# Kernel tuning notes

Hardware: AMD Instinct MI355X
Metric: run time of the kernel (lower is better)

The kernel has to match this reference:

```python
import jax, jax.numpy as jnp
import numpy as np

B, S, T, H, E = 64, 256, 128, 1024, 512


def setup_inputs() -> dict:
    key = jax.random.key(0)
    ks = jax.random.split(key, 16)
    sc = 0.02
    inp = {
        "trg_embed": jax.random.normal(ks[0], (B, T, E), jnp.float32),
        "encoder_hidden": jax.random.normal(ks[1], (B, S, 2 * H), jnp.float32),
        "encoder_final": jax.random.normal(ks[2], (1, B, 2 * H), jnp.float32),
        "src_mask": jnp.ones((B, 1, S), dtype=bool),
        "trg_mask": jnp.ones((B, 1, T), dtype=bool),
        # bridge: Linear(2H -> H, bias)
        "W_bridge": jax.random.normal(ks[3], (H, 2 * H), jnp.float32) * sc,
        "b_bridge": jnp.zeros((H,), jnp.float32),
        # Bahdanau attention: key/query/energy layers (no bias)
        "W_key": jax.random.normal(ks[4], (H, 2 * H), jnp.float32) * sc,
        "W_query": jax.random.normal(ks[5], (H, H), jnp.float32) * sc,
        "v_energy": jax.random.normal(ks[6], (H,), jnp.float32) * sc,
        # GRU (1 layer): input size E + 2H, hidden H. PyTorch gate order [r, z, n].
        "W_ih": jax.random.normal(ks[7], (3 * H, E + 2 * H), jnp.float32) * sc,
        "W_hh": jax.random.normal(ks[8], (3 * H, H), jnp.float32) * sc,
        "b_ih": jnp.zeros((3 * H,), jnp.float32),
        "b_hh": jnp.zeros((3 * H,), jnp.float32),
        # pre_output: Linear(H + 2H + E -> H, no bias)
        "W_pre": jax.random.normal(ks[9], (H, H + 2 * H + E), jnp.float32) * sc,
    }
    return inp


def reference(trg_embed, encoder_hidden, encoder_final, src_mask, trg_mask,
              W_bridge, b_bridge, W_key, W_query, v_energy,
              W_ih, W_hh, b_ih, b_hh, W_pre):
    neg_inf = jnp.float32(-1e9)
    # init_hidden: tanh(bridge(encoder_final)) -> [num_layers, B, H]; take last layer
    h0 = jnp.tanh(jnp.einsum('lbk,hk->lbh', encoder_final, W_bridge) + b_bridge)[-1]  # [B, H]
    # precompute projected keys once (as in forward())
    proj_key = jnp.einsum('bsk,hk->bsh', encoder_hidden, W_key)  # [B, S, H]
    mask = src_mask[:, 0, :]  # [B, S]

    def step(h, prev_embed):  # h: [B,H], prev_embed: [B,E]
        # Bahdanau attention with query = last-layer hidden state
        q = h @ W_query.T                                        # [B, H]
        energies = jnp.tanh(q[:, None, :] + proj_key) @ v_energy  # [B, S]
        energies = jnp.where(mask, energies, neg_inf)
        alphas = jax.nn.softmax(energies, axis=-1)               # [B, S]
        context = jnp.einsum('bs,bsd->bd', alphas, encoder_hidden)  # [B, 2H]
        # GRU step on concat(prev_embed, context)
        x = jnp.concatenate([prev_embed, context], axis=-1)      # [B, E+2H]
        gi = x @ W_ih.T + b_ih                                   # [B, 3H]
        gh = h @ W_hh.T + b_hh                                   # [B, 3H]
        i_r, i_z, i_n = jnp.split(gi, 3, axis=-1)
        h_r, h_z, h_n = jnp.split(gh, 3, axis=-1)
        r = jax.nn.sigmoid(i_r + h_r)
        z = jax.nn.sigmoid(i_z + h_z)
        n = jnp.tanh(i_n + r * h_n)
        h_new = (1.0 - z) * n + z * h                            # [B, H]
        # pre-output projection (dropout disabled: eval / p effectively identity)
        pre = jnp.concatenate([prev_embed, h_new, context], axis=-1) @ W_pre.T  # [B, H]
        return h_new, (h_new, pre)

    h_final, (states, pres) = jax.lax.scan(step, h0, jnp.swapaxes(trg_embed, 0, 1))
    decoder_states = jnp.swapaxes(states, 0, 1)      # [B, T, H]
    pre_output_vectors = jnp.swapaxes(pres, 0, 1)    # [B, T, H]
    hidden = h_final[None]                            # [num_layers=1, B, H]
    return decoder_states, hidden, pre_output_vectors
```

## Files before the change

kernel.cpp:

```cpp
#include <hip/hip_runtime.h>

#define Bn 64
#define Sn 256
#define Tn 128
#define Hn 1024
#define En 512
#define H2n 2048
#define NBLK 256
#define NTHR 1024

#define WCTX 10
#define WH 12

#define GW 0
#define PWc 0
#define PWh 32768
#define PWq 49152
#define PWe 65536
#define PREP 73728
#define SCR2 75776
#define SCR 147456
#define GIL 155648
#define LDS_BYTES 161792

typedef __attribute__((ext_vector_type(8))) short short8v;
typedef __attribute__((ext_vector_type(4))) float floatx4;

__device__ __forceinline__ unsigned short f2bf(float f) {
  union { float f; unsigned u; } x; x.f = f;
  unsigned r = x.u + 0x7fffu + ((x.u >> 16) & 1u);
  return (unsigned short)(r >> 16);
}
__device__ __forceinline__ float bf2f(unsigned short u) {
  union { unsigned u; float f; } x; x.u = ((unsigned)u) << 16; return x.f;
}
__device__ __forceinline__ float sigm(float x) { return 1.f / (1.f + __expf(-x)); }
__device__ __forceinline__ float tanh_f(float x) {
  float e = __expf(2.f * x);
  return 1.f - 2.f / (e + 1.f);
}
__device__ __forceinline__ short8v ldf(const unsigned short* p) { return *(const short8v*)p; }
#define MFMA(a, b, c) __builtin_amdgcn_mfma_f32_16x16x32_bf16(a, b, c, 0, 0, 0)

__device__ __forceinline__ float ldc_f(const float* p) {
  return __hip_atomic_load(p, __ATOMIC_RELAXED, __HIP_MEMORY_SCOPE_AGENT);
}
__device__ __forceinline__ void stc_f(float* p, float v) {
  __hip_atomic_store(p, v, __ATOMIC_RELAXED, __HIP_MEMORY_SCOPE_AGENT);
}
__device__ __forceinline__ void stc_u32(unsigned* p, unsigned v) {
  __hip_atomic_store(p, v, __ATOMIC_RELAXED, __HIP_MEMORY_SCOPE_AGENT);
}
__device__ __forceinline__ unsigned long long ldc_u64(const unsigned long long* p) {
  return __hip_atomic_load(p, __ATOMIC_RELAXED, __HIP_MEMORY_SCOPE_AGENT);
}
__device__ __forceinline__ void stc_u64(unsigned long long* p, unsigned long long v) {
  __hip_atomic_store(p, v, __ATOMIC_RELAXED, __HIP_MEMORY_SCOPE_AGENT);
}

__device__ __forceinline__ void bar_lds() {
  __builtin_amdgcn_sched_barrier(0);
  asm volatile("s_waitcnt lgkmcnt(0)" ::: "memory");
  __builtin_amdgcn_s_barrier();
  __builtin_amdgcn_sched_barrier(0);
}

__device__ __forceinline__ short8v packf(const float* p) {
  float4 e0 = *(const float4*)p, e1 = *(const float4*)(p + 4);
  short8v x;
  x[0] = (short)f2bf(e0.x); x[1] = (short)f2bf(e0.y);
  x[2] = (short)f2bf(e0.z); x[3] = (short)f2bf(e0.w);
  x[4] = (short)f2bf(e1.x); x[5] = (short)f2bf(e1.y);
  x[6] = (short)f2bf(e1.z); x[7] = (short)f2bf(e1.w);
  return x;
}

__global__ __launch_bounds__(256) void cast_kernel(const float4* __restrict__ src,
                                                   uint2* __restrict__ dst, int n4) {
  for (int i = blockIdx.x * blockDim.x + threadIdx.x; i < n4; i += gridDim.x * blockDim.x) {
    float4 v = src[i];
    uint2 p;
    p.x = (unsigned)f2bf(v.x) | ((unsigned)f2bf(v.y) << 16);
    p.y = (unsigned)f2bf(v.z) | ((unsigned)f2bf(v.w) << 16);
    dst[i] = p;
  }
}

__global__ __launch_bounds__(256) void bridge_kernel(const float* __restrict__ ef,
                                                     const float* __restrict__ Wb,
                                                     const float* __restrict__ bb,
                                                     float* __restrict__ h0out,
                                                     unsigned short* __restrict__ hb0) {
  __shared__ float efs[H2n];
  const int b = blockIdx.x >> 2, jq = blockIdx.x & 3;
  const int j = jq * 256 + threadIdx.x;
  for (int i = threadIdx.x; i < H2n; i += 256) efs[i] = ef[(size_t)b * H2n + i];
  __syncthreads();
  const float* wr = Wb + (size_t)j * H2n;
  float acc = bb[j];
  for (int k = 0; k < H2n; k += 4) {
    float4 wv = *(const float4*)&wr[k];
    acc += efs[k] * wv.x + efs[k + 1] * wv.y + efs[k + 2] * wv.z + efs[k + 3] * wv.w;
  }
  float th = tanhf(acc);
  h0out[(size_t)b * Hn + j] = th;
  hb0[(size_t)b * Hn + j] = f2bf(th);
}

__global__ __launch_bounds__(256) void pk_gemm(const unsigned short* __restrict__ A,
                                               const unsigned short* __restrict__ Bw,
                                               unsigned short* __restrict__ pk) {
  const int bid = blockIdx.x;
  const int mt = bid >> 4, nt = bid & 15;
  const int w = threadIdx.x >> 6, lane = threadIdx.x & 63;
  const int lm = lane & 15, lk = lane >> 4, ko = lk * 8;
  const unsigned short* arow = A + (size_t)(mt * 64 + w * 16 + lm) * 2048 + ko;
  const unsigned short* b0 = Bw + (size_t)(nt * 64 + lm) * 2048 + ko;
  const unsigned short* b1 = Bw + (size_t)(nt * 64 + 16 + lm) * 2048 + ko;
  const unsigned short* b2 = Bw + (size_t)(nt * 64 + 32 + lm) * 2048 + ko;
  const unsigned short* b3 = Bw + (size_t)(nt * 64 + 48 + lm) * 2048 + ko;
  floatx4 c0 = {0,0,0,0}, c1 = {0,0,0,0}, c2 = {0,0,0,0}, c3 = {0,0,0,0};
  for (int k = 0; k < 2048; k += 32) {
    short8v a = ldf(arow + k);
    c0 = MFMA(a, ldf(b0 + k), c0);
    c1 = MFMA(a, ldf(b1 + k), c1);
    c2 = MFMA(a, ldf(b2 + k), c2);
    c3 = MFMA(a, ldf(b3 + k), c3);
  }
  const int m = mt * 64 + w * 16 + lk * 4;
  const int j = nt * 64 + lm;
#pragma unroll
  for (int r = 0; r < 4; ++r) {
    unsigned short* row = pk + (size_t)(m + r) * 1024 + j;
    row[0]  = f2bf(c0[r]);
    row[16] = f2bf(c1[r]);
    row[32] = f2bf(c2[r]);
    row[48] = f2bf(c3[r]);
  }
}

struct DA {
  const float* emb; const float* v; const float* bih; const float* bhh;
  const unsigned short* pk; const unsigned short* ehb;
  const unsigned short* Wih; const unsigned short* Whh;
  const unsigned short* Wpre; const unsigned short* Wq;
  float* hbuf; unsigned short* hbR; float* qbuf; float* wbuf; float* psump;
  unsigned short* ctxR; unsigned* bar; float* out;
};

__device__ __forceinline__ void gbar(unsigned* bar, int tid, unsigned idx, int inv) {
  asm volatile("s_waitcnt vmcnt(0)" ::: "memory");
  __syncthreads();
  if (tid == 0) {
    unsigned old = __hip_atomic_fetch_add(bar, 1u, __ATOMIC_RELAXED, __HIP_MEMORY_SCOPE_AGENT);
    if (old + 1u == (unsigned)NBLK * idx) {
      __hip_atomic_store(bar + 32, idx, __ATOMIC_RELAXED, __HIP_MEMORY_SCOPE_AGENT);
    } else {
      unsigned g;
      do {
        __builtin_amdgcn_s_sleep(2);
        g = __hip_atomic_load(bar + 32, __ATOMIC_RELAXED, __HIP_MEMORY_SCOPE_AGENT);
      } while (g < idx);
    }
  }
  __syncthreads();
  if (inv) __builtin_amdgcn_fence(__ATOMIC_ACQUIRE, "agent");
}

__device__ __forceinline__ void gbar_pk(const DA& a, unsigned* bar, int tid, unsigned idx,
                                        int inv, int b, int sc4, int w, int lane,
                                        short8v* pkr) {
  asm volatile("s_waitcnt vmcnt(0)" ::: "memory");
  __syncthreads();
  __builtin_amdgcn_sched_barrier(0);
#pragma unroll
  for (int i = 0; i < 4; ++i) {
    const unsigned short* prow =
        a.pk + ((size_t)b * Sn + sc4 * 64 + w * 4 + i) * Hn + lane * 16;
    pkr[i] = ldf(prow);
    pkr[4 + i] = ldf(prow + 8);
  }
  __builtin_amdgcn_sched_barrier(0);
  if (tid == 0) {
    unsigned old = __hip_atomic_fetch_add(bar, 1u, __ATOMIC_RELAXED, __HIP_MEMORY_SCOPE_AGENT);
    if (old + 1u == (unsigned)NBLK * idx) {
      __hip_atomic_store(bar + 32, idx, __ATOMIC_RELAXED, __HIP_MEMORY_SCOPE_AGENT);
    } else {
      unsigned g;
      do {
        __builtin_amdgcn_s_sleep(2);
        g = __hip_atomic_load(bar + 32, __ATOMIC_RELAXED, __HIP_MEMORY_SCOPE_AGENT);
      } while (g < idx);
    }
  }
  __syncthreads();
  if (inv) __builtin_amdgcn_fence(__ATOMIC_ACQUIRE, "agent");
}

__device__ __forceinline__ void gateC_signal(unsigned* bar, int tid) {
  asm volatile("s_waitcnt vmcnt(0)" ::: "memory");
  __syncthreads();
  if (tid == 0)
    __hip_atomic_fetch_add(bar + 512, 1u, __ATOMIC_RELAXED, __HIP_MEMORY_SCOPE_AGENT);
}
__device__ __forceinline__ void gateC_wait(unsigned* bar, int tid, unsigned tgt) {
  __syncthreads();
  if (tid == 0) {
    while (__hip_atomic_load(bar + 512, __ATOMIC_RELAXED, __HIP_MEMORY_SCOPE_AGENT) < tgt)
      __builtin_amdgcn_s_sleep(1);
  }
  __syncthreads();
}

__device__ __forceinline__ void preD_wait_pk(const DA& a, unsigned* bar, int tid,
                                             unsigned tgt, int inv, int isGate,
                                             int b, int sc4, int w, int lane,
                                             short8v* pkr) {
  if (!isGate) {
    asm volatile("s_waitcnt vmcnt(0)" ::: "memory");
    __syncthreads();
    if (tid == 0)
      __hip_atomic_fetch_add(bar + 544, 1u, __ATOMIC_RELAXED, __HIP_MEMORY_SCOPE_AGENT);
  } else {
    __syncthreads();
  }
  __builtin_amdgcn_sched_barrier(0);
#pragma unroll
  for (int i = 0; i < 4; ++i) {
    const unsigned short* prow =
        a.pk + ((size_t)b * Sn + sc4 * 64 + w * 4 + i) * Hn + lane * 16;
    pkr[i] = ldf(prow);
    pkr[4 + i] = ldf(prow + 8);
  }
  __builtin_amdgcn_sched_barrier(0);
  if (tid == 0) {
    while (__hip_atomic_load(bar + 544, __ATOMIC_RELAXED, __HIP_MEMORY_SCOPE_AGENT) < tgt)
      __builtin_amdgcn_s_sleep(1);
  }
  __syncthreads();
  if (inv) __builtin_amdgcn_fence(__ATOMIC_ACQUIRE, "agent");
}

__device__ __forceinline__ void phA(const DA& a, char* dsm, int bid, int tid,
                                    int w, int lane, int t, const short8v* pkr) {
  const int b = bid >> 2, sc4 = bid & 3;
  float* w_s = (float*)(dsm + SCR);
  float* q_s = (float*)(dsm + SCR + 1024);
  if (tid < 256) {
    const unsigned long long* qp = (const unsigned long long*)(a.qbuf + (size_t)b * Hn) + tid * 2;
    unsigned long long u0 = ldc_u64(qp), u1 = ldc_u64(qp + 1);
    union { unsigned long long u; float f[2]; } x0, x1; x0.u = u0; x1.u = u1;
    q_s[tid * 4] = x0.f[0]; q_s[tid * 4 + 1] = x0.f[1];
    q_s[tid * 4 + 2] = x1.f[0]; q_s[tid * 4 + 3] = x1.f[1];
  }
  __syncthreads();
  float qr[16], vr[16];
  const float* vp = a.v + lane * 16;
#pragma unroll
  for (int i = 0; i < 16; i += 4) {
    *(float4*)&qr[i] = *(const float4*)&q_s[lane * 16 + i];
    *(float4*)&vr[i] = *(const float4*)(vp + i);
  }
#pragma unroll
  for (int i = 0; i < 4; ++i) {
    float ep = 0.f;
#pragma unroll
    for (int e = 0; e < 8; ++e) {
      ep += vr[e] * tanh_f(qr[e] + bf2f((unsigned short)pkr[i][e]));
      ep += vr[8 + e] * tanh_f(qr[8 + e] + bf2f((unsigned short)pkr[4 + i][e]));
    }
#pragma unroll
    for (int m = 1; m < 64; m <<= 1) ep += __shfl_xor(ep, m, 64);
    if (lane == 0) {
      float wv = __expf(ep - 20.f);
      w_s[w * 4 + i] = wv;
      stc_f(a.wbuf + (size_t)b * Sn + sc4 * 64 + w * 4 + i, wv);
    }
  }
  const int ls = lane >> 2, ldcx = lane & 3;
  const int dchunk = w * 4 + ldcx;
  const unsigned short* ebase = a.ehb + (size_t)b * Sn * H2n + sc4 * 512 + dchunk * 8;
  short8v er[8];
#pragma unroll
  for (int k = 0; k < 8; ++k) er[k] = ldf(ebase + (size_t)(ls + k * 16) * H2n);
  bar_lds();
  if (tid < 64) {
    float wv = w_s[tid];
#pragma unroll
    for (int m = 1; m < 64; m <<= 1) wv += __shfl_xor(wv, m, 64);
    if (tid == 0) stc_f(a.psump + sc4 * 64 + b, wv);
  }
  asm volatile("s_waitcnt vmcnt(0)" ::: "memory");
  __syncthreads();
  if (tid == 0) stc_u32(&a.bar[64 + (b << 2) + sc4], (unsigned)(t + 1));
  if (tid < 4) {
    while (__hip_atomic_load(&a.bar[64 + (b << 2) + tid], __ATOMIC_RELAXED,
                             __HIP_MEMORY_SCOPE_AGENT) < (unsigned)(t + 1))
      __builtin_amdgcn_s_sleep(1);
  }
  __syncthreads();
  float* wn = (float*)(dsm + SCR);
  float psinv = 1.f / (ldc_f(a.psump + b) + ldc_f(a.psump + 64 + b) +
                       ldc_f(a.psump + 128 + b) + ldc_f(a.psump + 192 + b));
  if (tid < 256) wn[tid] = ldc_f(a.wbuf + (size_t)b * Sn + tid) * psinv;
  __syncthreads();
  float acc[8] = {};
#pragma unroll
  for (int k = 0; k < 8; ++k) {
    float wf = wn[ls + k * 16];
#pragma unroll
    for (int e2 = 0; e2 < 8; ++e2) acc[e2] += wf * bf2f((unsigned short)er[k][e2]);
  }
#pragma unroll
  for (int k = 8; k < 16; ++k) {
    short8v e = ldf(ebase + (size_t)(ls + k * 16) * H2n);
    float wf = wn[ls + k * 16];
#pragma unroll
    for (int e2 = 0; e2 < 8; ++e2) acc[e2] += wf * bf2f((unsigned short)e[e2]);
  }
#pragma unroll
  for (int m = 4; m < 64; m <<= 1) {
#pragma unroll
    for (int e2 = 0; e2 < 8; ++e2) acc[e2] += __shfl_xor(acc[e2], m, 64);
  }
  if (ls == 0) {
    union { unsigned long long u[2]; unsigned short s[8]; } p;
#pragma unroll
    for (int e2 = 0; e2 < 8; ++e2) p.s[e2] = f2bf(acc[e2]);
    unsigned long long* dst = (unsigned long long*)(
        a.ctxR + (size_t)(t % WCTX) * Bn * H2n + (size_t)b * H2n + sc4 * 512 + dchunk * 8);
    stc_u64(dst, p.u[0]); stc_u64(dst + 1, p.u[1]);
  }
}

__device__ __forceinline__ void gate_c(const DA& a, char* dsm, int j0, int w,
                                       int lane, int tid, int t, int cur, int nxt) {
  float* scr = (float*)(dsm + SCR);
  for (int i = tid; i < 2048; i += NTHR) scr[i] = 0.f;
  __syncthreads();
  const int mt = w & 3, ks = w >> 2;
  const int lm = lane & 15, lk = lane >> 4;
  const int arow = mt * 16 + lm, jb = lm & 7;
  const unsigned short* ctxrow =
      a.ctxR + (size_t)(t % WCTX) * Bn * H2n + (size_t)arow * H2n + lk * 8;
  const unsigned short* hrow =
      a.hbR + (size_t)(t % WH) * Bn * Hn + (size_t)arow * Hn + lk * 8;
  const char* wb0 = dsm + GW + (size_t)((0 * 8 + jb) * 384) * 16;
  const char* wb1 = dsm + GW + (size_t)((1 * 8 + jb) * 384) * 16;
  const char* wb2 = dsm + GW + (size_t)((2 * 8 + jb) * 384) * 16;
  floatx4 ar = {0,0,0,0}, az = {0,0,0,0}, ain = {0,0,0,0}, ahn = {0,0,0,0};
#pragma unroll 4
  for (int kc = ks * 24; kc < ks * 24 + 24; ++kc) {
    short8v x = (kc < 64) ? ldf(ctxrow + kc * 32) : ldf(hrow + (kc - 64) * 32);
    const size_t slot = (size_t)((kc * 4 + lk) ^ jb) * 16;
    ar = MFMA(x, *(const short8v*)(wb0 + slot), ar);
    az = MFMA(x, *(const short8v*)(wb1 + slot), az);
    if (kc < 64) ain = MFMA(x, *(const short8v*)(wb2 + slot), ain);
    else         ahn = MFMA(x, *(const short8v*)(wb2 + slot), ahn);
  }
  if (lm < 8) {
#pragma unroll
    for (int r = 0; r < 4; ++r) {
      const int bb = mt * 16 + lk * 4 + r;
      atomicAdd(&scr[(0 * 64 + bb) * 8 + jb], ar[r]);
      atomicAdd(&scr[(1 * 64 + bb) * 8 + jb], az[r]);
      atomicAdd(&scr[(2 * 64 + bb) * 8 + jb], ain[r]);
      atomicAdd(&scr[(3 * 64 + bb) * 8 + jb], ahn[r]);
    }
  }
  __syncthreads();
  if (tid < 256) {
    const int bb = tid >> 2, jj = (tid & 3) * 2;
    float* gil = (float*)(dsm + GIL);
    float hn2[2];
#pragma unroll
    for (int u = 0; u < 2; ++u) {
      const int j = jj + u, jg = j0 + j;
      float grv = scr[(0 * 64 + bb) * 8 + j] + gil[(0 * 64 + bb) * 8 + j] + a.bhh[jg];
      float gzv = scr[(1 * 64 + bb) * 8 + j] + gil[(1 * 64 + bb) * 8 + j] + a.bhh[Hn + jg];
      float ginv = scr[(2 * 64 + bb) * 8 + j] + gil[(2 * 64 + bb) * 8 + j];
      float ghnv = scr[(3 * 64 + bb) * 8 + j] + a.bhh[2 * Hn + jg];
      float rr = sigm(grv), zz = sigm(gzv);
      float nn = tanh_f(ginv + rr * ghnv);
      float hold = a.hbuf[(size_t)cur * Bn * Hn + (size_t)bb * Hn + jg];
      float hnew = (1.f - zz) * nn + zz * hold;
      hn2[u] = hnew;
      a.hbuf[(size_t)nxt * Bn * Hn + (size_t)bb * Hn + jg] = hnew;
      a.out[((size_t)bb * Tn + t) * Hn + jg] = hnew;
      if (t == Tn - 1) a.out[(size_t)Bn * Tn * Hn + (size_t)bb * Hn + jg] = hnew;
    }
    unsigned hpack = (unsigned)f2bf(hn2[0]) | ((unsigned)f2bf(hn2[1]) << 16);
    stc_u32((unsigned*)(a.hbR + (size_t)((t + 1) % WH) * Bn * Hn +
                        (size_t)bb * Hn + j0 + jj), hpack);
  }
}

__device__ __forceinline__ void pre_c(const DA& a, char* dsm, int j0, int w,
                                      int lane, int tid, int t) {
  float* prep = (float*)(dsm + PREP);
  for (int i = tid; i < 512; i += NTHR) prep[i] = 0.f;
  __syncthreads();
  const int mt = w & 3, ks = w >> 2;
  const int lm = lane & 15, lk = lane >> 4;
  const int arow = mt * 16 + lm, jb = lm & 7;
  const unsigned short* ctxrow =
      a.ctxR + (size_t)(t % WCTX) * Bn * H2n + (size_t)arow * H2n + lk * 8;
  const float* ep = a.emb + ((size_t)arow * Tn + t) * En + lk * 8;
  const char* we = dsm + PWe + (size_t)(jb * 64) * 16;
  const char* wc = dsm + PWc + (size_t)(jb * 256) * 16;
  floatx4 acc = {0,0,0,0};
#pragma unroll 4
  for (int kc = ks * 20; kc < ks * 20 + 20; ++kc) {
    if (kc < 16) {
      acc = MFMA(packf(ep + kc * 32),
                 *(const short8v*)(we + (size_t)((kc * 4 + lk) ^ jb) * 16), acc);
    } else {
      const int c = kc - 16;
      acc = MFMA(ldf(ctxrow + c * 32),
                 *(const short8v*)(wc + (size_t)((c * 4 + lk) ^ jb) * 16), acc);
    }
  }
  if (lm < 8) {
#pragma unroll
    for (int r = 0; r < 4; ++r)
      atomicAdd(&prep[(mt * 16 + lk * 4 + r) * 8 + jb], acc[r]);
  }
  __syncthreads();
}

__device__ __forceinline__ void pre_d(const DA& a, char* dsm, int j0, int w,
                                      int lane, int tid, int t, int hslot, int doPre) {
  float* scr = (float*)(dsm + SCR2);
  for (int i = tid; i < 1024; i += NTHR) scr[i] = 0.f;
  __syncthreads();
  const int mt = w & 3, part = w >> 2;
  const int lm = lane & 15, lk = lane >> 4;
  const int arow = mt * 16 + lm, jb = lm & 7;
  const unsigned short* hrow =
      a.hbR + (size_t)hslot * Bn * Hn + (size_t)arow * Hn + lk * 8;
  const int isQ = part >> 1;
  const char* wbase = dsm + (isQ ? PWq : PWh) + (size_t)(jb * 128) * 16;
  if (doPre || isQ) {
    floatx4 acc = {0,0,0,0};
    const int k0 = (part & 1) * 16;
#pragma unroll 4
    for (int kh = k0; kh < k0 + 16; ++kh)
      acc = MFMA(ldf(hrow + kh * 32),
                 *(const short8v*)(wbase + (size_t)((kh * 4 + lk) ^ jb) * 16), acc);
    if (lm < 8) {
#pragma unroll
      for (int r = 0; r < 4; ++r)
        atomicAdd(&scr[(isQ * 64 + mt * 16 + lk * 4 + r) * 8 + jb], acc[r]);
    }
  }
  __syncthreads();
  if (tid < 256) {
    const int bb = tid >> 2, jj = (tid & 3) * 2;
    float* prep = (float*)(dsm + PREP);
#pragma unroll
    for (int u = 0; u < 2; ++u) {
      const int j = jj + u, jg = j0 + j;
      if (doPre) {
        float pv = scr[(0 * 64 + bb) * 8 + j] + prep[bb * 8 + j];
        a.out[(size_t)Bn * Tn * Hn + (size_t)Bn * Hn + ((size_t)bb * Tn + t) * Hn + jg] = pv;
      }
      stc_f(a.qbuf + (size_t)bb * Hn + jg, scr[(1 * 64 + bb) * 8 + j]);
    }
  }
}

__device__ __forceinline__ void gi_compute(const DA& a, char* dsm, int j0, int w,
                                           int lane, int t1) {
  const int mt = w & 3, g = w >> 2;
  if (g >= 3) return;
  const int lm = lane & 15, lk = lane >> 4;
  const int arow = mt * 16 + lm;
  const unsigned short* wrow = a.Wih + (size_t)(g * Hn + j0 + (lm & 7)) * 2560 + lk * 8;
  const float* ep = a.emb + ((size_t)arow * Tn + t1) * En + lk * 8;
  floatx4 acc = {0,0,0,0};
#pragma unroll 4
  for (int kk = 0; kk < 16; ++kk)
    acc = MFMA(packf(ep + kk * 32), ldf(wrow + kk * 32), acc);
  if (lm < 8) {
    float* gil = (float*)(dsm + GIL);
    float bv = a.bih[g * Hn + j0 + lm];
#pragma unroll
    for (int r = 0; r < 4; ++r)
      gil[(g * 64 + mt * 16 + lk * 4 + r) * 8 + lm] = acc[r] + bv;
  }
}

__global__ void __attribute__((amdgpu_flat_work_group_size(1024, 1024),
                               amdgpu_waves_per_eu(4, 4)))
dec_kernel(DA a) {
  extern __shared__ char dsm[];
  const int tid = threadIdx.x, bid = blockIdx.x;
  const int w = tid >> 6, lane = tid & 63;
  const bool isGate = bid < 128;
  const int j0 = (isGate ? bid : bid - 128) * 8;
  const int pb = bid >> 2, psc4 = bid & 3;

  if (isGate) {
    for (int idx = tid; idx < 9216; idx += NTHR) {
      int row = idx / 384, c = idx % 384;
      int g = row >> 3, j = row & 7;
      const unsigned short* src = (c < 256)
          ? a.Wih + (size_t)(g * Hn + j0 + j) * 2560 + 512 + c * 8
          : a.Whh + (size_t)(g * Hn + j0 + j) * Hn + (c - 256) * 8;
      *(uint4*)(dsm + (size_t)(row * 384 + (c ^ j)) * 16) = *(const uint4*)src;
    }
  } else {
    for (int idx = tid; idx < 4608; idx += NTHR) {
      const unsigned short* src; size_t dst;
      if (idx < 2048) {
        int j = idx >> 8, c = idx & 255;
        src = a.Wpre + (size_t)(j0 + j) * 3584 + 1536 + c * 8;
        dst = PWc + (size_t)(j * 256 + (c ^ j)) * 16;
      } else if (idx < 3072) {
        int i = idx - 2048, j = i >> 7, c = i & 127;
        src = a.Wpre + (size_t)(j0 + j) * 3584 + 512 + c * 8;
        dst = PWh + (size_t)(j * 128 + (c ^ j)) * 16;
      } else if (idx < 4096) {
        int i = idx - 3072, j = i >> 7, c = i & 127;
        src = a.Wq + (size_t)(j0 + j) * Hn + c * 8;
        dst = PWq + (size_t)(j * 128 + (c ^ j)) * 16;
      } else {
        int i = idx - 4096, j = i >> 6, c = i & 63;
        src = a.Wpre + (size_t)(j0 + j) * 3584 + c * 8;
        dst = PWe + (size_t)(j * 64 + (c ^ j)) * 16;
      }
      *(uint4*)(dsm + dst) = *(const uint4*)src;
    }
  }
  __syncthreads();

  short8v pkr[8];
  unsigned bi = 1;
  if (isGate) gi_compute(a, dsm, j0, w, lane, 0);
  else pre_d(a, dsm, j0, w, lane, tid, 0, 0, 0);
  gbar_pk(a, a.bar, tid, bi++, 0, pb, psc4, w, lane, pkr);

  for (int t = 0; t < Tn; ++t) {
    const int cur = t & 1, nxt = cur ^ 1;
    phA(a, dsm, bid, tid, w, lane, t, pkr);
    gbar(a.bar, tid, bi++, 0);
    if (isGate) {
      gate_c(a, dsm, j0, w, lane, tid, t, cur, nxt);
      gateC_signal(a.bar, tid);
      if (t + 1 < Tn) gi_compute(a, dsm, j0, w, lane, t + 1);
    } else {
      pre_c(a, dsm, j0, w, lane, tid, t);
      gateC_wait(a.bar, tid, 128u * (unsigned)(t + 1));
      pre_d(a, dsm, j0, w, lane, tid, t, (t + 1) % WH, 1);
    }
    preD_wait_pk(a, a.bar, tid, 128u * (unsigned)(t + 1), (t & 7) == 7,
                 isGate, pb, psc4, w, lane, pkr);
  }
}

extern "C" void kernel_launch(void* const* d_in, const int* in_sizes, int n_in,
                              void* d_out, int out_size, void* d_ws, size_t ws_size,
                              hipStream_t stream) {
  (void)in_sizes; (void)n_in; (void)out_size; (void)ws_size;
  const float* emb = (const float*)d_in[0];
  const float* eh  = (const float*)d_in[1];
  const float* ef  = (const float*)d_in[2];
  const float* Wb  = (const float*)d_in[5];
  const float* bb  = (const float*)d_in[6];
  const float* Wk  = (const float*)d_in[7];
  const float* Wq  = (const float*)d_in[8];
  const float* v   = (const float*)d_in[9];
  const float* Wih = (const float*)d_in[10];
  const float* Whh = (const float*)d_in[11];
  const float* bih = (const float*)d_in[12];
  const float* bhh = (const float*)d_in[13];
  const float* Wpre= (const float*)d_in[14];
  float* out = (float*)d_out;

  char* wsb = (char*)d_ws;
  unsigned short* ehb  = (unsigned short*)(wsb + 0);
  unsigned short* pkb  = (unsigned short*)(wsb + 67108864);
  unsigned short* Wihb = (unsigned short*)(wsb + 100663296);
  unsigned short* Whhb = (unsigned short*)(wsb + 116391936);
  unsigned short* Wpreb= (unsigned short*)(wsb + 122683392);
  unsigned short* Wqb  = (unsigned short*)(wsb + 130023424);
  unsigned short* Wkb  = (unsigned short*)(wsb + 132120576);
  unsigned short* ctxR = (unsigned short*)(wsb + 132120576);
  unsigned short* hbR  = (unsigned short*)(wsb + 134742016);
  float* hbuf = (float*)(wsb + 136314880);
  float* qbuf = (float*)(wsb + 137101312);
  float* wbuf = (float*)(wsb + 137363456);
  float* psump= (float*)(wsb + 137428992);
  unsigned* bar = (unsigned*)(wsb + 137695232);

  hipMemsetAsync(bar, 0, 4096, stream);
  cast_kernel<<<2048, 256, 0, stream>>>((const float4*)eh, (uint2*)ehb, Bn * Sn * H2n / 4);
  cast_kernel<<<2048, 256, 0, stream>>>((const float4*)Wih, (uint2*)Wihb, 3 * Hn * 2560 / 4);
  cast_kernel<<<1024, 256, 0, stream>>>((const float4*)Whh, (uint2*)Whhb, 3 * Hn * Hn / 4);
  cast_kernel<<<1024, 256, 0, stream>>>((const float4*)Wpre, (uint2*)Wpreb, Hn * 3584 / 4);
  cast_kernel<<<512, 256, 0, stream>>>((const float4*)Wq, (uint2*)Wqb, Hn * Hn / 4);
  cast_kernel<<<512, 256, 0, stream>>>((const float4*)Wk, (uint2*)Wkb, Hn * H2n / 4);
  pk_gemm<<<4096, 256, 0, stream>>>(ehb, Wkb, pkb);
  bridge_kernel<<<256, 256, 0, stream>>>(ef, Wb, bb, hbuf, hbR);

  DA da;
  da.emb = emb; da.v = v; da.bih = bih; da.bhh = bhh;
  da.pk = pkb; da.ehb = ehb;
  da.Wih = Wihb; da.Whh = Whhb; da.Wpre = Wpreb; da.Wq = Wqb;
  da.hbuf = hbuf; da.hbR = hbR; da.qbuf = qbuf; da.wbuf = wbuf; da.psump = psump;
  da.ctxR = ctxR; da.bar = bar; da.out = out;

  hipFuncSetAttribute(reinterpret_cast<const void*>(&dec_kernel),
                      hipFuncAttributeMaxDynamicSharedMemorySize, LDS_BYTES);
  void* kp[] = { (void*)&da };
  hipLaunchCooperativeKernel(reinterpret_cast<const void*>(&dec_kernel),
                             dim3(NBLK), dim3(NTHR), kp, LDS_BYTES, stream);
}
```

Measured before the change: 10.97 ms.

## Store projected keys in FP8 and keep non-gate blocks' slice resident in LDS

Projected keys are now quantised to an FP8 E4M3-like format in the precompute GEMM instead of bf16, halving the bytes streamed per attention step. Non-gate blocks copy their 64x1024 key slice into LDS once at startup and read it from shared memory every step. Gate blocks still reload from global memory at each barrier. This cuts per-step global traffic for the attention energies, at the cost of extra software decode ALU work and reduced precision in the energies.

```diff
diff --git a/kernel.cpp b/kernel.cpp
--- a/kernel.cpp
+++ b/kernel.cpp
@@ -19,6 +19,7 @@
 #define PWe 65536
 #define PREP 73728
 #define SCR2 75776
+#define PKL 81920
 #define SCR 147456
 #define GIL 155648
 #define LDS_BYTES 161792
@@ -41,6 +42,24 @@
 }
 __device__ __forceinline__ short8v ldf(const unsigned short* p) { return *(const short8v*)p; }
 #define MFMA(a, b, c) __builtin_amdgcn_mfma_f32_16x16x32_bf16(a, b, c, 0, 0, 0)
+
+__device__ __forceinline__ unsigned char f2fp8z(float f) {
+  union { float f; unsigned u; } x; x.f = f;
+  unsigned s = (x.u >> 24) & 0x80u;
+  unsigned au = x.u & 0x7fffffffu;
+  if (au >= 0x43e00000u) return (unsigned char)(s | 0x7Eu);
+  if (au < 0x3c000000u) return (unsigned char)s;
+  if (au < 0x3c800000u) return (unsigned char)(s | 0x08u);
+  unsigned r = au + 0x7ffffu + ((au >> 20) & 1u);
+  unsigned e8 = ((r >> 23) & 0xffu) - 120u;
+  unsigned m8 = (r >> 20) & 7u;
+  return (unsigned char)(s | (e8 << 3) | m8);
+}
+__device__ __forceinline__ float dec1(unsigned b) {
+  union { unsigned u; float f; } x;
+  x.u = ((b & 0x80u) << 24) | ((b & 0x7fu) << 20);
+  return x.f * 0x1p120f;
+}
 
 __device__ __forceinline__ float ldc_f(const float* p) {
   return __hip_atomic_load(p, __ATOMIC_RELAXED, __HIP_MEMORY_SCOPE_AGENT);
@@ -109,7 +128,7 @@
 
 __global__ __launch_bounds__(256) void pk_gemm(const unsigned short* __restrict__ A,
                                                const unsigned short* __restrict__ Bw,
-                                               unsigned short* __restrict__ pk) {
+                                               unsigned char* __restrict__ pk8) {
   const int bid = blockIdx.x;
   const int mt = bid >> 4, nt = bid & 15;
   const int w = threadIdx.x >> 6, lane = threadIdx.x & 63;
@@ -131,17 +150,17 @@
   const int j = nt * 64 + lm;
 #pragma unroll
   for (int r = 0; r < 4; ++r) {
-    unsigned short* row = pk + (size_t)(m + r) * 1024 + j;
-    row[0]  = f2bf(c0[r]);
-    row[16] = f2bf(c1[r]);
-    row[32] = f2bf(c2[r]);
-    row[48] = f2bf(c3[r]);
+    unsigned char* row = pk8 + (size_t)(m + r) * 1024 + j;
+    row[0]  = f2fp8z(c0[r]);
+    row[16] = f2fp8z(c1[r]);
+    row[32] = f2fp8z(c2[r]);
+    row[48] = f2fp8z(c3[r]);
   }
 }
 
 struct DA {
   const float* emb; const float* v; const float* bih; const float* bhh;
-  const unsigned short* pk; const unsigned short* ehb;
+  const unsigned char* pk8; const unsigned short* ehb;
   const unsigned short* Wih; const unsigned short* Whh;
   const unsigned short* Wpre; const unsigned short* Wq;
   float* hbuf; unsigned short* hbR; float* qbuf; float* wbuf; float* psump;
@@ -168,17 +187,18 @@
 }
 
 __device__ __forceinline__ void gbar_pk(const DA& a, unsigned* bar, int tid, unsigned idx,
-                                        int inv, int b, int sc4, int w, int lane,
-                                        short8v* pkr) {
+                                        int inv, int isGate, int b, int sc4, int w,
+                                        int lane, uint4* pkr8) {
   asm volatile("s_waitcnt vmcnt(0)" ::: "memory");
   __syncthreads();
   __builtin_amdgcn_sched_barrier(0);
-#pragma unroll
-  for (int i = 0; i < 4; ++i) {
-    const unsigned short* prow =
-        a.pk + ((size_t)b * Sn + sc4 * 64 + w * 4 + i) * Hn + lane * 16;
-    pkr[i] = ldf(prow);
-    pkr[4 + i] = ldf(prow + 8);
+  if (isGate) {
+#pragma unroll
+    for (int i = 0; i < 4; ++i) {
+      const unsigned char* prow =
+          a.pk8 + ((size_t)b * Sn + sc4 * 64 + w * 4 + i) * 1024 + lane * 16;
+      pkr8[i] = *(const uint4*)prow;
+    }
   }
   __builtin_amdgcn_sched_barrier(0);
   if (tid == 0) {
@@ -215,7 +235,7 @@
 __device__ __forceinline__ void preD_wait_pk(const DA& a, unsigned* bar, int tid,
                                              unsigned tgt, int inv, int isGate,
                                              int b, int sc4, int w, int lane,
-                                             short8v* pkr) {
+                                             uint4* pkr8) {
   if (!isGate) {
     asm volatile("s_waitcnt vmcnt(0)" ::: "memory");
     __syncthreads();
@@ -225,12 +245,13 @@
     __syncthreads();
   }
   __builtin_amdgcn_sched_barrier(0);
-#pragma unroll
-  for (int i = 0; i < 4; ++i) {
-    const unsigned short* prow =
-        a.pk + ((size_t)b * Sn + sc4 * 64 + w * 4 + i) * Hn + lane * 16;
-    pkr[i] = ldf(prow);
-    pkr[4 + i] = ldf(prow + 8);
+  if (isGate) {
+#pragma unroll
+    for (int i = 0; i < 4; ++i) {
+      const unsigned char* prow =
+          a.pk8 + ((size_t)b * Sn + sc4 * 64 + w * 4 + i) * 1024 + lane * 16;
+      pkr8[i] = *(const uint4*)prow;
+    }
   }
   __builtin_amdgcn_sched_barrier(0);
   if (tid == 0) {
@@ -242,7 +263,7 @@
 }
 
 __device__ __forceinline__ void phA(const DA& a, char* dsm, int bid, int tid,
-                                    int w, int lane, int t, const short8v* pkr) {
+                                    int w, int lane, int t, uint4* pkr8, int isGate) {
   const int b = bid >> 2, sc4 = bid & 3;
   float* w_s = (float*)(dsm + SCR);
   float* q_s = (float*)(dsm + SCR + 1024);
@@ -254,6 +275,11 @@
     q_s[tid * 4 + 2] = x1.f[0]; q_s[tid * 4 + 3] = x1.f[1];
   }
   __syncthreads();
+  if (!isGate) {
+#pragma unroll
+    for (int i = 0; i < 4; ++i)
+      pkr8[i] = *(const uint4*)(dsm + PKL + (size_t)(w * 4 + i) * 1024 + lane * 16);
+  }
   float qr[16], vr[16];
   const float* vp = a.v + lane * 16;
 #pragma unroll
@@ -264,10 +290,13 @@
 #pragma unroll
   for (int i = 0; i < 4; ++i) {
     float ep = 0.f;
-#pragma unroll
-    for (int e = 0; e < 8; ++e) {
-      ep += vr[e] * tanh_f(qr[e] + bf2f((unsigned short)pkr[i][e]));
-      ep += vr[8 + e] * tanh_f(qr[8 + e] + bf2f((unsigned short)pkr[4 + i][e]));
+    unsigned pw0 = pkr8[i].x, pw1 = pkr8[i].y, pw2 = pkr8[i].z, pw3 = pkr8[i].w;
+#pragma unroll
+    for (int k = 0; k < 4; ++k) {
+      ep += vr[k]      * tanh_f(qr[k]      + dec1((pw0 >> (8 * k)) & 0xffu));
+      ep += vr[4 + k]  * tanh_f(qr[4 + k]  + dec1((pw1 >> (8 * k)) & 0xffu));
+      ep += vr[8 + k]  * tanh_f(qr[8 + k]  + dec1((pw2 >> (8 * k)) & 0xffu));
+      ep += vr[12 + k] * tanh_f(qr[12 + k] + dec1((pw3 >> (8 * k)) & 0xffu));
     }
 #pragma unroll
     for (int m = 1; m < 64; m <<= 1) ep += __shfl_xor(ep, m, 64);
@@ -531,18 +560,21 @@
       }
       *(uint4*)(dsm + dst) = *(const uint4*)src;
     }
-  }
-  __syncthreads();
-
-  short8v pkr[8];
+    const unsigned char* ps = a.pk8 + ((size_t)pb * Sn + psc4 * 64) * 1024;
+    for (int idx = tid; idx < 4096; idx += NTHR)
+      *(uint4*)(dsm + PKL + (size_t)idx * 16) = *(const uint4*)(ps + (size_t)idx * 16);
+  }
+  __syncthreads();
+
+  uint4 pkr8[4];
   unsigned bi = 1;
   if (isGate) gi_compute(a, dsm, j0, w, lane, 0);
   else pre_d(a, dsm, j0, w, lane, tid, 0, 0, 0);
-  gbar_pk(a, a.bar, tid, bi++, 0, pb, psc4, w, lane, pkr);
+  gbar_pk(a, a.bar, tid, bi++, 0, isGate, pb, psc4, w, lane, pkr8);
 
   for (int t = 0; t < Tn; ++t) {
     const int cur = t & 1, nxt = cur ^ 1;
-    phA(a, dsm, bid, tid, w, lane, t, pkr);
+    phA(a, dsm, bid, tid, w, lane, t, pkr8, isGate);
     gbar(a.bar, tid, bi++, 0);
     if (isGate) {
       gate_c(a, dsm, j0, w, lane, tid, t, cur, nxt);
@@ -554,7 +586,7 @@
       pre_d(a, dsm, j0, w, lane, tid, t, (t + 1) % WH, 1);
     }
     preD_wait_pk(a, a.bar, tid, 128u * (unsigned)(t + 1), (t & 7) == 7,
-                 isGate, pb, psc4, w, lane, pkr);
+                 isGate, pb, psc4, w, lane, pkr8);
   }
 }
 
@@ -579,19 +611,19 @@
 
   char* wsb = (char*)d_ws;
   unsigned short* ehb  = (unsigned short*)(wsb + 0);
-  unsigned short* pkb  = (unsigned short*)(wsb + 67108864);
-  unsigned short* Wihb = (unsigned short*)(wsb + 100663296);
-  unsigned short* Whhb = (unsigned short*)(wsb + 116391936);
-  unsigned short* Wpreb= (unsigned short*)(wsb + 122683392);
-  unsigned short* Wqb  = (unsigned short*)(wsb + 130023424);
-  unsigned short* Wkb  = (unsigned short*)(wsb + 132120576);
-  unsigned short* ctxR = (unsigned short*)(wsb + 132120576);
-  unsigned short* hbR  = (unsigned short*)(wsb + 134742016);
-  float* hbuf = (float*)(wsb + 136314880);
-  float* qbuf = (float*)(wsb + 137101312);
-  float* wbuf = (float*)(wsb + 137363456);
-  float* psump= (float*)(wsb + 137428992);
-  unsigned* bar = (unsigned*)(wsb + 137695232);
+  unsigned char*  pk8  = (unsigned char*)(wsb + 67108864);
+  unsigned short* Wihb = (unsigned short*)(wsb + 83886080);
+  unsigned short* Whhb = (unsigned short*)(wsb + 99614720);
+  unsigned short* Wpreb= (unsigned short*)(wsb + 105906176);
+  unsigned short* Wqb  = (unsigned short*)(wsb + 113246208);
+  unsigned short* Wkb  = (unsigned short*)(wsb + 115343360);
+  unsigned short* ctxR = (unsigned short*)(wsb + 115343360);
+  unsigned short* hbR  = (unsigned short*)(wsb + 117964800);
+  float* hbuf = (float*)(wsb + 119537664);
+  float* qbuf = (float*)(wsb + 120061952);
+  float* wbuf = (float*)(wsb + 120324096);
+  float* psump= (float*)(wsb + 120389632);
+  unsigned* bar = (unsigned*)(wsb + 120393728);
 
   hipMemsetAsync(bar, 0, 4096, stream);
   cast_kernel<<<2048, 256, 0, stream>>>((const float4*)eh, (uint2*)ehb, Bn * Sn * H2n / 4);
@@ -600,12 +632,12 @@
   cast_kernel<<<1024, 256, 0, stream>>>((const float4*)Wpre, (uint2*)Wpreb, Hn * 3584 / 4);
   cast_kernel<<<512, 256, 0, stream>>>((const float4*)Wq, (uint2*)Wqb, Hn * Hn / 4);
   cast_kernel<<<512, 256, 0, stream>>>((const float4*)Wk, (uint2*)Wkb, Hn * H2n / 4);
-  pk_gemm<<<4096, 256, 0, stream>>>(ehb, Wkb, pkb);
+  pk_gemm<<<4096, 256, 0, stream>>>(ehb, Wkb, pk8);
   bridge_kernel<<<256, 256, 0, stream>>>(ef, Wb, bb, hbuf, hbR);
 
   DA da;
   da.emb = emb; da.v = v; da.bih = bih; da.bhh = bhh;
-  da.pk = pkb; da.ehb = ehb;
+  da.pk8 = pk8; da.ehb = ehb;
   da.Wih = Wihb; da.Whh = Whhb; da.Wpre = Wpreb; da.Wq = Wqb;
   da.hbuf = hbuf; da.hbR = hbR; da.qbuf = qbuf; da.wbuf = wbuf; da.psump = psump;
   da.ctxR = ctxR; da.bar = bar; da.out = out;
```

Result: no change. 11.14 ms (+1.5%).
